# Kernel tuning notes

Hardware: AMD Instinct MI355X
Metric: run time of the kernel (lower is better)

## Reference

```python
import jax, jax.numpy as jnp
import numpy as np

# dims: M scalars (0e), K vectors (1e) in input; T = tp_features; N = batch of atoms
M, K, T, N = 128, 64, 64, 131072
D_IN = M + 3 * K  # 320, e3nn layout: [128x0e | 64x1e flattened as (mul, 3)]


def _act_norm(f):
    # e3nn Activation normalizes act so E_{z~N(0,1)}[act(z)^2] = 1
    z = np.linspace(-8.0, 8.0, 20001)
    pdf = np.exp(-0.5 * z * z) / np.sqrt(2.0 * np.pi)
    return float(np.sqrt(np.trapz(f(z) ** 2 * pdf, z)))

C_SILU = _act_norm(lambda z: z / (1.0 + np.exp(-z)))
C_RELU = _act_norm(lambda z: np.maximum(z, 0.0))
INV_SQRT_M = float(1.0 / np.sqrt(M))
INV_SQRT_K = float(1.0 / np.sqrt(K))
INV_SQRT_3 = float(1.0 / np.sqrt(3.0))  # wigner_3j(1,1,0) = delta_ij/sqrt(3)
TP_NORM = float(1.0 / np.sqrt(2.0 * T * T))  # fan-in over the 2 paths into 0e


def setup_inputs() -> dict:
    key = jax.random.key(0)
    ks = jax.random.split(key, 11)
    f32 = jnp.float32
    return {
        "x": jax.random.normal(ks[0], (N, D_IN), f32),
        "input_shift": jnp.zeros((D_IN,), f32),
        "output_scale": jnp.ones((), f32),
        # PerceptronLayer 1: Linear (Mx0e+Kx1e) -> ((M+K)x0e + Kx1e)
        "w0_1": jax.random.normal(ks[1], (M, M + K), f32),
        "b0_1": jnp.zeros((M + K,), f32),
        "w1_1": jax.random.normal(ks[2], (K, K), f32),
        # PerceptronLayer 2 (same irreps, resnet applies)
        "w0_2": jax.random.normal(ks[3], (M, M + K), f32),
        "b0_2": jnp.zeros((M + K,), f32),
        "w1_2": jax.random.normal(ks[4], (K, K), f32),
        # linear_out: (Mx0e+Kx1e) -> (Tx0e+Tx1e)
        "w0_o": jax.random.normal(ks[5], (M, T), f32),
        "b0_o": jnp.zeros((T,), f32),
        "w1_o": jax.random.normal(ks[6], (K, T), f32),
        # FullyConnectedTensorProduct (tp, tp) -> 1x0e: paths 0e*0e->0e, 1e*1e->0e
        "w_tp0": jax.random.normal(ks[7], (T, T), f32),
        "w_tp1": jax.random.normal(ks[8], (T, T), f32),
    }


def _linear(xs, xv, w0, b0, w1):
    # e3nn o3.Linear: per-irrep dense mixing with 1/sqrt(fan_in), bias on 0e only
    ys = xs @ w0 * INV_SQRT_M + b0          # [N, M+K] scalars + gates
    yv = jnp.einsum('nki,kj->nji', xv, w1) * INV_SQRT_K  # [N, K, 3]
    return ys, yv


def _gate(ys, yv):
    # e3nn Gate: silu on 0e scalars, relu on 0e gates, gate the 1e vectors
    s = jax.nn.silu(ys[:, :M]) / C_SILU     # [N, M]
    g = jax.nn.relu(ys[:, M:]) / C_RELU     # [N, K]
    return s, yv * g[:, :, None]


def reference(x, input_shift, output_scale,
              w0_1, b0_1, w1_1, w0_2, b0_2, w1_2,
              w0_o, b0_o, w1_o, w_tp0, w_tp1):
    x = x - input_shift
    xs = x[:, :M]                           # [N, M] 0e block
    xv = x[:, M:].reshape(-1, K, 3)         # [N, K, 3] 1e block
    for (w0, b0, w1) in ((w0_1, b0_1, w1_1), (w0_2, b0_2, w1_2)):
        ys, yv = _linear(xs, xv, w0, b0, w1)
        s, v = _gate(ys, yv)
        xs = xs + s                         # resnet: irreps_in == irreps_out
        xv = xv + v
    # linear_out -> irreps_tp = Tx0e + Tx1e
    zs = xs @ w0_o * INV_SQRT_M + b0_o                    # [N, T]
    zv = jnp.einsum('nki,kj->nji', xv, w1_o) * INV_SQRT_K # [N, T, 3]
    # FullyConnectedTensorProduct(z, z) -> 0e (avoid [N,T,T] blowup)
    y0 = jnp.sum((zs @ w_tp0) * zs, axis=-1)                                    # [N]
    y1 = jnp.sum(jnp.einsum('nui,uv->nvi', zv, w_tp1) * zv, axis=(1, 2)) * INV_SQRT_3
    y = (y0 + y1) * TP_NORM / output_scale
    return y[:, None]
```

## Files before the change

kernel.cpp:

```cpp
#include <hip/hip_runtime.h>
#include <math.h>


typedef _Float16 f16;
typedef _Float16 f16x8 __attribute__((ext_vector_type(8)));
typedef __fp16   fp16x2 __attribute__((ext_vector_type(2)));
typedef float    f32x4 __attribute__((ext_vector_type(4)));
typedef int      i32x4 __attribute__((ext_vector_type(4)));

#define MFMA16(a, b, c) __builtin_amdgcn_mfma_f32_16x16x32_f16(a, b, c, 0, 0, 0)

constexpr float INV_SQRT_M = 0.08838834764831845f;
constexpr float INV_SQRT_K = 0.125f;
constexpr float INV_SQRT_3 = 0.57735026918962576f;
constexpr float TP_NORM    = 0.011048543456039806f;

#define OFF_W01 0
#define OFF_W11 24576
#define OFF_W02 28672
#define OFF_W12 53248
#define OFF_W0O 57344
#define OFF_W1O 65536
#define OFF_TP0 69632
#define OFF_TP1 73728
#define PACK_UNITS 9728

#define LDS_W1   24576
#define LDS_W0O  0
#define LDS_W1O  8192
#define LDS_TP0  12288
#define LDS_TP1  16384

#define NTHR 512

__global__ void init_consts_kernel(float* __restrict__ ws) {
    __shared__ double red[256];
    const int t = threadIdx.x;
    double acc_s = 0.0, acc_r = 0.0;
    for (int i = t; i <= 20000; i += 256) {
        const double z = -8.0 + (16.0 * (double)i) / 20000.0;
        const double pdf = exp(-0.5 * z * z) / 2.5066282746310002;
        const double sil = z / (1.0 + exp(-z));
        const double wgt = (i == 0 || i == 20000) ? 0.5 : 1.0;
        acc_s += wgt * sil * sil * pdf;
        if (z > 0.0) acc_r += wgt * z * z * pdf;
    }
    red[t] = acc_s;
    __syncthreads();
    for (int o = 128; o > 0; o >>= 1) { if (t < o) red[t] += red[t + o]; __syncthreads(); }
    const double tot_s = red[0];
    __syncthreads();
    red[t] = acc_r;
    __syncthreads();
    for (int o = 128; o > 0; o >>= 1) { if (t < o) red[t] += red[t + o]; __syncthreads(); }
    if (t == 0) {
        const double dz = 16.0 / 20000.0;
        ws[0] = (float)(1.0 / sqrt(tot_s * dz));
        ws[1] = (float)(1.0 / sqrt(red[0] * dz));
    }
}

__global__ void pack_weights(const float* __restrict__ w01, const float* __restrict__ w11,
                             const float* __restrict__ w02, const float* __restrict__ w12,
                             const float* __restrict__ w0o, const float* __restrict__ w1o,
                             const float* __restrict__ tp0, const float* __restrict__ tp1,
                             f16* __restrict__ dst) {
    int u = blockIdx.x * 256 + threadIdx.x;
    if (u >= PACK_UNITS) return;
    const float* src; int NC, base, lu = u; float sc;
    if      (lu < 3072) {            src = w01; NC = 192; base = OFF_W01; sc = INV_SQRT_M; }
    else if (lu < 3584) { lu -= 3072; src = w11; NC = 64;  base = OFF_W11; sc = INV_SQRT_K; }
    else if (lu < 6656) { lu -= 3584; src = w02; NC = 192; base = OFF_W02; sc = INV_SQRT_M; }
    else if (lu < 7168) { lu -= 6656; src = w12; NC = 64;  base = OFF_W12; sc = INV_SQRT_K; }
    else if (lu < 8192) { lu -= 7168; src = w0o; NC = 64;  base = OFF_W0O; sc = INV_SQRT_M; }
    else if (lu < 8704) { lu -= 8192; src = w1o; NC = 64;  base = OFF_W1O; sc = INV_SQRT_K; }
    else if (lu < 9216) { lu -= 8704; src = tp0; NC = 64;  base = OFF_TP0; sc = 1.0f; }
    else                { lu -= 9216; src = tp1; NC = 64;  base = OFF_TP1; sc = INV_SQRT_3; }
    const int lane = lu & 63;
    const int frag = lu >> 6;
    const int NT = NC >> 4;
    const int kstep = frag / NT, nj = frag - kstep * NT;
    const int gl  = lane >> 4;
    const int col = nj * 16 + (lane & 15);
    f16 tmp[8];
    #pragma unroll
    for (int e = 0; e < 8; ++e) {
        const int row = kstep * 32 + ((e >> 2) << 4) + (gl << 2) + (e & 3);
        tmp[e] = (f16)(src[(size_t)row * NC + col] * sc);
    }
    *(f16x8*)&dst[(size_t)(base) + (size_t)lu * 8] = *(f16x8*)tmp;
}

__device__ __forceinline__ int pk2i(float a, float b) {
    union { fp16x2 h; int i; } u;
    u.h = __builtin_amdgcn_cvt_pkrtz(a, b);
    return u.i;
}

__device__ __forceinline__ f16x8 packB(f32x4 t0, f32x4 t1) {
    union { i32x4 i; f16x8 v; } u;
    u.i[0] = pk2i(t0[0], t0[1]);
    u.i[1] = pk2i(t0[2], t0[3]);
    u.i[2] = pk2i(t1[0], t1[1]);
    u.i[3] = pk2i(t1[2], t1[3]);
    return u.v;
}

union Frag { f16x8 v; fp16x2 h2[4]; };

__device__ __forceinline__ void resblock32(
    Frag (&xsS)[2][4], Frag (&xvS)[2][3][2],
    const f16* lds, const float* __restrict__ b0,
    float invCS, float invCR, int l, int g)
{
    f16x8 xsB[2][4];
    #pragma unroll
    for (int h = 0; h < 2; ++h)
        #pragma unroll
        for (int ks = 0; ks < 4; ++ks)
            xsB[h][ks] = xsS[h][ks].v;

    float gate[2][4][4];
    #pragma unroll
    for (int nj = 0; nj < 12; ++nj) {
        f32x4 acc0 = {0.f, 0.f, 0.f, 0.f}, acc1 = {0.f, 0.f, 0.f, 0.f};
        #pragma unroll
        for (int ks = 0; ks < 4; ++ks) {
            const f16x8 a = *(const f16x8*)&lds[(size_t)((ks * 12 + nj) * 64 + l) * 8];
            acc0 = MFMA16(a, xsB[0][ks], acc0);
            acc1 = MFMA16(a, xsB[1][ks], acc1);
        }
        const f32x4 bias = *(const f32x4*)(b0 + nj * 16 + g * 4);
        #pragma unroll
        for (int h = 0; h < 2; ++h) {
            const f32x4 acc = h ? acc1 : acc0;
            if (nj < 8) {
                float s[4];
                #pragma unroll
                for (int r = 0; r < 4; ++r) {
                    const float ys = acc[r] + bias[r];
                    s[r] = ys * __builtin_amdgcn_rcpf(1.0f + __expf(-ys)) * invCS;
                }
                xsS[h][nj >> 1].h2[2 * (nj & 1)]     += __builtin_amdgcn_cvt_pkrtz(s[0], s[1]);
                xsS[h][nj >> 1].h2[2 * (nj & 1) + 1] += __builtin_amdgcn_cvt_pkrtz(s[2], s[3]);
            } else {
                #pragma unroll
                for (int r = 0; r < 4; ++r) {
                    const float ys = acc[r] + bias[r];
                    gate[h][nj - 8][r] = fmaxf(ys, 0.f) * invCR;
                }
            }
        }
    }

    f16x8 xvB[2][3][2];
    #pragma unroll
    for (int h = 0; h < 2; ++h)
        #pragma unroll
        for (int i = 0; i < 3; ++i)
            #pragma unroll
            for (int ks = 0; ks < 2; ++ks)
                xvB[h][i][ks] = xvS[h][i][ks].v;

    #pragma unroll
    for (int i = 0; i < 3; ++i)
        #pragma unroll
        for (int nj = 0; nj < 4; ++nj) {
            f32x4 acc0 = {0.f, 0.f, 0.f, 0.f}, acc1 = {0.f, 0.f, 0.f, 0.f};
            #pragma unroll
            for (int ks = 0; ks < 2; ++ks) {
                const f16x8 a = *(const f16x8*)&lds[LDS_W1 + (size_t)((ks * 4 + nj) * 64 + l) * 8];
                acc0 = MFMA16(a, xvB[0][i][ks], acc0);
                acc1 = MFMA16(a, xvB[1][i][ks], acc1);
            }
            #pragma unroll
            for (int h = 0; h < 2; ++h) {
                const f32x4 acc = h ? acc1 : acc0;
                float u[4];
                #pragma unroll
                for (int r = 0; r < 4; ++r)
                    u[r] = acc[r] * gate[h][nj][r];
                xvS[h][i][nj >> 1].h2[2 * (nj & 1)]     += __builtin_amdgcn_cvt_pkrtz(u[0], u[1]);
                xvS[h][i][nj >> 1].h2[2 * (nj & 1) + 1] += __builtin_amdgcn_cvt_pkrtz(u[2], u[3]);
            }
        }
}

__global__ __launch_bounds__(NTHR, 2)
void corrnet_lds(const float* __restrict__ x, const float* __restrict__ shift,
                 const float* __restrict__ oscale,
                 const float* __restrict__ b01, const float* __restrict__ b02,
                 const float* __restrict__ b0o,
                 const f16* __restrict__ wp, const float* __restrict__ consts,
                 float* __restrict__ out)
{
    __shared__ __align__(16) f16 smem[3584 * 8];

    const int t = threadIdx.x;
    const int l = t & 63;
    const int w = __builtin_amdgcn_readfirstlane(t >> 6);
    const int g = l >> 4;
    const int c = l & 15;
    const size_t n0 = (size_t)blockIdx.x * 256 + (size_t)w * 32;

    const float invCS = consts[0], invCR = consts[1];
    const float inv_os = 1.0f / oscale[0];

    #pragma unroll
    for (int it = 0; it < 7; ++it) {
        const int u = it * NTHR + t;
        *(f16x8*)&smem[(size_t)u * 8] = *(const f16x8*)&wp[(size_t)u * 8];
    }

    Frag xsS[2][4];
    Frag xvS[2][3][2];
    #pragma unroll
    for (int h = 0; h < 2; ++h) {
        const float* xrow = x + (n0 + h * 16 + c) * 320;
        #pragma unroll
        for (int ks = 0; ks < 4; ++ks) {
            const int col = ks * 32 + g * 4;
            const f32x4 t0 = *(const f32x4*)(xrow + col)      - *(const f32x4*)(shift + col);
            const f32x4 t1 = *(const f32x4*)(xrow + col + 16) - *(const f32x4*)(shift + col + 16);
            xsS[h][ks].v = packB(t0, t1);
        }
        f32x4 tmp[3][4];
        #pragma unroll
        for (int tau = 0; tau < 4; ++tau) {
            const int col = 128 + 3 * (tau * 16 + g * 4);
            const f32x4 a0 = *(const f32x4*)(xrow + col)     - *(const f32x4*)(shift + col);
            const f32x4 a1 = *(const f32x4*)(xrow + col + 4) - *(const f32x4*)(shift + col + 4);
            const f32x4 a2 = *(const f32x4*)(xrow + col + 8) - *(const f32x4*)(shift + col + 8);
            float arr[12];
            #pragma unroll
            for (int e = 0; e < 4; ++e) {
                arr[e] = a0[e]; arr[4 + e] = a1[e]; arr[8 + e] = a2[e];
            }
            #pragma unroll
            for (int r = 0; r < 4; ++r)
                #pragma unroll
                for (int i = 0; i < 3; ++i)
                    tmp[i][tau][r] = arr[3 * r + i];
        }
        #pragma unroll
        for (int i = 0; i < 3; ++i)
            #pragma unroll
            for (int ks = 0; ks < 2; ++ks)
                xvS[h][i][ks].v = packB(tmp[i][2 * ks], tmp[i][2 * ks + 1]);
    }

    __syncthreads();
    resblock32(xsS, xvS, smem, b01, invCS, invCR, l, g);
    __syncthreads();

    #pragma unroll
    for (int it = 0; it < 7; ++it) {
        const int u = it * NTHR + t;
        *(f16x8*)&smem[(size_t)u * 8] = *(const f16x8*)&wp[(size_t)(OFF_W02) + (size_t)u * 8];
    }
    __syncthreads();
    resblock32(xsS, xvS, smem, b02, invCS, invCR, l, g);
    __syncthreads();

    #pragma unroll
    for (int it = 0; it < 5; ++it) {
        const int u = it * NTHR + t;
        *(f16x8*)&smem[(size_t)u * 8] = *(const f16x8*)&wp[(size_t)(OFF_W0O) + (size_t)u * 8];
    }
    __syncthreads();

    f32x4 zs[2][4];
    #pragma unroll
    for (int nj = 0; nj < 4; ++nj) {
        f32x4 acc0 = {0.f, 0.f, 0.f, 0.f}, acc1 = {0.f, 0.f, 0.f, 0.f};
        #pragma unroll
        for (int ks = 0; ks < 4; ++ks) {
            const f16x8 a = *(const f16x8*)&smem[LDS_W0O + (size_t)((ks * 4 + nj) * 64 + l) * 8];
            acc0 = MFMA16(a, xsS[0][ks].v, acc0);
            acc1 = MFMA16(a, xsS[1][ks].v, acc1);
        }
        const f32x4 bias = *(const f32x4*)(b0o + nj * 16 + g * 4);
        #pragma unroll
        for (int r = 0; r < 4; ++r) {
            zs[0][nj][r] = acc0[r] + bias[r];
            zs[1][nj][r] = acc1[r] + bias[r];
        }
    }

    float part[2]  = {0.f, 0.f};
    float part1[2] = {0.f, 0.f};

    {
        f16x8 zsB[2][2];
        #pragma unroll
        for (int h = 0; h < 2; ++h)
            #pragma unroll
            for (int ks = 0; ks < 2; ++ks)
                zsB[h][ks] = packB(zs[h][2 * ks], zs[h][2 * ks + 1]);
        #pragma unroll
        for (int nj = 0; nj < 4; ++nj) {
            f32x4 acc0 = {0.f, 0.f, 0.f, 0.f}, acc1 = {0.f, 0.f, 0.f, 0.f};
            #pragma unroll
            for (int ks = 0; ks < 2; ++ks) {
                const f16x8 a = *(const f16x8*)&smem[LDS_TP0 + (size_t)((ks * 4 + nj) * 64 + l) * 8];
                acc0 = MFMA16(a, zsB[0][ks], acc0);
                acc1 = MFMA16(a, zsB[1][ks], acc1);
            }
            #pragma unroll
            for (int r = 0; r < 4; ++r) {
                part[0] += acc0[r] * zs[0][nj][r];
                part[1] += acc1[r] * zs[1][nj][r];
            }
        }
    }

    #pragma unroll
    for (int i = 0; i < 3; ++i) {
        f32x4 zv[2][4];
        #pragma unroll
        for (int nj = 0; nj < 4; ++nj) {
            f32x4 acc0 = {0.f, 0.f, 0.f, 0.f}, acc1 = {0.f, 0.f, 0.f, 0.f};
            #pragma unroll
            for (int ks = 0; ks < 2; ++ks) {
                const f16x8 a = *(const f16x8*)&smem[LDS_W1O + (size_t)((ks * 4 + nj) * 64 + l) * 8];
                acc0 = MFMA16(a, xvS[0][i][ks].v, acc0);
                acc1 = MFMA16(a, xvS[1][i][ks].v, acc1);
            }
            #pragma unroll
            for (int r = 0; r < 4; ++r) {
                zv[0][nj][r] = acc0[r];
                zv[1][nj][r] = acc1[r];
            }
        }
        f16x8 zvB[2][2];
        #pragma unroll
        for (int h = 0; h < 2; ++h)
            #pragma unroll
            for (int ks = 0; ks < 2; ++ks)
                zvB[h][ks] = packB(zv[h][2 * ks], zv[h][2 * ks + 1]);
        #pragma unroll
        for (int nj = 0; nj < 4; ++nj) {
            f32x4 acc0 = {0.f, 0.f, 0.f, 0.f}, acc1 = {0.f, 0.f, 0.f, 0.f};
            #pragma unroll
            for (int ks = 0; ks < 2; ++ks) {
                const f16x8 a = *(const f16x8*)&smem[LDS_TP1 + (size_t)((ks * 4 + nj) * 64 + l) * 8];
                acc0 = MFMA16(a, zvB[0][ks], acc0);
                acc1 = MFMA16(a, zvB[1][ks], acc1);
            }
            #pragma unroll
            for (int r = 0; r < 4; ++r) {
                part1[0] += acc0[r] * zv[0][nj][r];
                part1[1] += acc1[r] * zv[1][nj][r];
            }
        }
    }
    #pragma unroll
    for (int h = 0; h < 2; ++h)
        part[h] += part1[h];

    #pragma unroll
    for (int h = 0; h < 2; ++h) {
        part[h] += __shfl_xor(part[h], 16, 64);
        part[h] += __shfl_xor(part[h], 32, 64);
    }

    if (l < 16)
        out[n0 + l] = part[0] * TP_NORM * inv_os;
    else if (l < 32)
        out[n0 + 16 + (l - 16)] = part[1] * TP_NORM * inv_os;
}

extern "C" void kernel_launch(void* const* d_in, const int* in_sizes, int n_in,
                              void* d_out, int out_size, void* d_ws, size_t ws_size,
                              hipStream_t stream) {
    const float* x      = (const float*)d_in[0];
    const float* shift  = (const float*)d_in[1];
    const float* oscale = (const float*)d_in[2];
    const float* w01    = (const float*)d_in[3];
    const float* b01    = (const float*)d_in[4];
    const float* w11    = (const float*)d_in[5];
    const float* w02    = (const float*)d_in[6];
    const float* b02    = (const float*)d_in[7];
    const float* w12    = (const float*)d_in[8];
    const float* w0o    = (const float*)d_in[9];
    const float* b0o    = (const float*)d_in[10];
    const float* w1o    = (const float*)d_in[11];
    const float* wtp0   = (const float*)d_in[12];
    const float* wtp1   = (const float*)d_in[13];
    float* out    = (float*)d_out;
    float* consts = (float*)d_ws;
    f16*   wp     = (f16*)((char*)d_ws + 16);

    init_consts_kernel<<<1, 256, 0, stream>>>(consts);
    pack_weights<<<(PACK_UNITS + 255) / 256, 256, 0, stream>>>(
        w01, w11, w02, w12, w0o, w1o, wtp0, wtp1, wp);

    const int nblocks = 131072 / 256;
    corrnet_lds<<<nblocks, NTHR, 0, stream>>>(
        x, shift, oscale, b01, b02, b0o, wp, consts, out);
}
```

Baseline: 91.13 us.

## Stage input rows through swizzled LDS with coalesced block-wide loads

Replaces per-lane strided global reads of x, where each lane read scattered 16-byte chunks of its own row, with a loop over 8 chunks of 32 rows. All 512 threads load each chunk into an XOR-swizzled LDS tile, and the owning wave then reads its fragments from LDS. This aims at full global-load coalescing and fewer wasted memory transactions. In exchange it serializes loading into 8 steps with two block barriers each, so only one wave consumes per step and global latency overlaps less.

```diff
diff --git a/kernel.cpp b/kernel.cpp
--- a/kernel.cpp
+++ b/kernel.cpp
@@ -32,6 +32,7 @@
 #define LDS_TP1  16384
 
 #define NTHR 512
+#define XSTR 324
 
 __global__ void init_consts_kernel(float* __restrict__ ws) {
     __shared__ double red[256];
@@ -195,60 +196,82 @@
                  float* __restrict__ out)
 {
     __shared__ __align__(16) f16 smem[3584 * 8];
+    float* smemF = (float*)smem;
 
     const int t = threadIdx.x;
     const int l = t & 63;
     const int w = __builtin_amdgcn_readfirstlane(t >> 6);
     const int g = l >> 4;
     const int c = l & 15;
-    const size_t n0 = (size_t)blockIdx.x * 256 + (size_t)w * 32;
+    const size_t nblk = (size_t)blockIdx.x * 256;
+    const size_t n0 = nblk + (size_t)w * 32;
 
     const float invCS = consts[0], invCR = consts[1];
     const float inv_os = 1.0f / oscale[0];
+
+    Frag xsS[2][4];
+    Frag xvS[2][3][2];
+    {
+        const int key = (c & 7) << 2;
+        #pragma unroll 1
+        for (int p = 0; p < 8; ++p) {
+            const float* xbase = x + (nblk + (size_t)p * 32) * 320;
+            #pragma unroll
+            for (int it = 0; it < 5; ++it) {
+                const int q    = it * NTHR + t;
+                const int row  = q / 80;
+                const int col4 = (q - row * 80) * 4;
+                const f32x4 v = *(const f32x4*)(xbase + row * 320 + col4)
+                              - *(const f32x4*)(shift + col4);
+                const int scol = col4 ^ ((row & 7) << 2);
+                *(f32x4*)&smemF[row * XSTR + scol] = v;
+            }
+            __syncthreads();
+            if (w == p) {
+                #pragma unroll
+                for (int h = 0; h < 2; ++h) {
+                    const int rbase = (h * 16 + c) * XSTR;
+                    #pragma unroll
+                    for (int ks = 0; ks < 4; ++ks) {
+                        const int col = ks * 32 + g * 4;
+                        const f32x4 t0 = *(const f32x4*)&smemF[rbase + (col ^ key)];
+                        const f32x4 t1 = *(const f32x4*)&smemF[rbase + ((col + 16) ^ key)];
+                        xsS[h][ks].v = packB(t0, t1);
+                    }
+                    f32x4 tmp[3][4];
+                    #pragma unroll
+                    for (int tau = 0; tau < 4; ++tau) {
+                        const int col0 = 128 + 3 * (tau * 16 + g * 4);
+                        const f32x4 a0 = *(const f32x4*)&smemF[rbase + (col0 ^ key)];
+                        const f32x4 a1 = *(const f32x4*)&smemF[rbase + ((col0 + 4) ^ key)];
+                        const f32x4 a2 = *(const f32x4*)&smemF[rbase + ((col0 + 8) ^ key)];
+                        float arr[12];
+                        #pragma unroll
+                        for (int e = 0; e < 4; ++e) {
+                            arr[e] = a0[e]; arr[4 + e] = a1[e]; arr[8 + e] = a2[e];
+                        }
+                        #pragma unroll
+                        for (int r = 0; r < 4; ++r)
+                            #pragma unroll
+                            for (int i = 0; i < 3; ++i)
+                                tmp[i][tau][r] = arr[3 * r + i];
+                    }
+                    #pragma unroll
+                    for (int i = 0; i < 3; ++i)
+                        #pragma unroll
+                        for (int ks = 0; ks < 2; ++ks)
+                            xvS[h][i][ks].v = packB(tmp[i][2 * ks], tmp[i][2 * ks + 1]);
+                }
+            }
+            __syncthreads();
+        }
+    }
 
     #pragma unroll
     for (int it = 0; it < 7; ++it) {
         const int u = it * NTHR + t;
         *(f16x8*)&smem[(size_t)u * 8] = *(const f16x8*)&wp[(size_t)u * 8];
     }
-
-    Frag xsS[2][4];
-    Frag xvS[2][3][2];
-    #pragma unroll
-    for (int h = 0; h < 2; ++h) {
-        const float* xrow = x + (n0 + h * 16 + c) * 320;
-        #pragma unroll
-        for (int ks = 0; ks < 4; ++ks) {
-            const int col = ks * 32 + g * 4;
-            const f32x4 t0 = *(const f32x4*)(xrow + col)      - *(const f32x4*)(shift + col);
-            const f32x4 t1 = *(const f32x4*)(xrow + col + 16) - *(const f32x4*)(shift + col + 16);
-            xsS[h][ks].v = packB(t0, t1);
-        }
-        f32x4 tmp[3][4];
-        #pragma unroll
-        for (int tau = 0; tau < 4; ++tau) {
-            const int col = 128 + 3 * (tau * 16 + g * 4);
-            const f32x4 a0 = *(const f32x4*)(xrow + col)     - *(const f32x4*)(shift + col);
-            const f32x4 a1 = *(const f32x4*)(xrow + col + 4) - *(const f32x4*)(shift + col + 4);
-            const f32x4 a2 = *(const f32x4*)(xrow + col + 8) - *(const f32x4*)(shift + col + 8);
-            float arr[12];
-            #pragma unroll
-            for (int e = 0; e < 4; ++e) {
-                arr[e] = a0[e]; arr[4 + e] = a1[e]; arr[8 + e] = a2[e];
-            }
-            #pragma unroll
-            for (int r = 0; r < 4; ++r)
-                #pragma unroll
-                for (int i = 0; i < 3; ++i)
-                    tmp[i][tau][r] = arr[3 * r + i];
-        }
-        #pragma unroll
-        for (int i = 0; i < 3; ++i)
-            #pragma unroll
-            for (int ks = 0; ks < 2; ++ks)
-                xvS[h][i][ks].v = packB(tmp[i][2 * ks], tmp[i][2 * ks + 1]);
-    }
-
     __syncthreads();
     resblock32(xsS, xvS, smem, b01, invCS, invCR, l, g);
     __syncthreads();
```

New measurement: 92.18 us. No clear change (+1.2%).

## Stage biases in LDS and widen constant-init kernel to 1024 threads

Applied to the files above, without the earlier changes.

Biases are packed into the workspace by the pack kernel and copied into shared memory alongside each weight stage, so the per-tile bias reads in the MFMA epilogues hit LDS instead of global memory. The init_consts kernel now uses 1024 threads, cutting its serial loop length. This adds a small LDS footprint and some extra copy instructions. The LDS bias region must not overlap the weight regions still in use.

```diff
diff --git a/kernel.cpp b/kernel.cpp
--- a/kernel.cpp
+++ b/kernel.cpp
@@ -24,20 +24,26 @@
 #define OFF_TP0 69632
 #define OFF_TP1 73728
 #define PACK_UNITS 9728
-
-#define LDS_W1   24576
-#define LDS_W0O  0
-#define LDS_W1O  8192
-#define LDS_TP0  12288
-#define LDS_TP1  16384
+#define FB01 38912
+#define FB02 39104
+#define FB0O 39296
+#define TOTAL_UNITS (PACK_UNITS + 448)
+
+#define LDS_W1     24576
+#define LDS_BIAS_F 14336
+#define LDS_W0O    0
+#define LDS_W1O    8192
+#define LDS_TP0    12288
+#define LDS_TP1    16384
+#define LDS_B0O_F  10240
 
 #define NTHR 512
 
 __global__ void init_consts_kernel(float* __restrict__ ws) {
-    __shared__ double red[256];
+    __shared__ double red[1024];
     const int t = threadIdx.x;
     double acc_s = 0.0, acc_r = 0.0;
-    for (int i = t; i <= 20000; i += 256) {
+    for (int i = t; i <= 20000; i += 1024) {
         const double z = -8.0 + (16.0 * (double)i) / 20000.0;
         const double pdf = exp(-0.5 * z * z) / 2.5066282746310002;
         const double sil = z / (1.0 + exp(-z));
@@ -47,12 +53,12 @@
     }
     red[t] = acc_s;
     __syncthreads();
-    for (int o = 128; o > 0; o >>= 1) { if (t < o) red[t] += red[t + o]; __syncthreads(); }
+    for (int o = 512; o > 0; o >>= 1) { if (t < o) red[t] += red[t + o]; __syncthreads(); }
     const double tot_s = red[0];
     __syncthreads();
     red[t] = acc_r;
     __syncthreads();
-    for (int o = 128; o > 0; o >>= 1) { if (t < o) red[t] += red[t + o]; __syncthreads(); }
+    for (int o = 512; o > 0; o >>= 1) { if (t < o) red[t] += red[t + o]; __syncthreads(); }
     if (t == 0) {
         const double dz = 16.0 / 20000.0;
         ws[0] = (float)(1.0 / sqrt(tot_s * dz));
@@ -64,9 +70,19 @@
                              const float* __restrict__ w02, const float* __restrict__ w12,
                              const float* __restrict__ w0o, const float* __restrict__ w1o,
                              const float* __restrict__ tp0, const float* __restrict__ tp1,
+                             const float* __restrict__ b01, const float* __restrict__ b02,
+                             const float* __restrict__ b0o,
                              f16* __restrict__ dst) {
     int u = blockIdx.x * 256 + threadIdx.x;
-    if (u >= PACK_UNITS) return;
+    if (u >= TOTAL_UNITS) return;
+    if (u >= PACK_UNITS) {
+        const int idx = u - PACK_UNITS;
+        float* dstF = (float*)dst;
+        if (idx < 192)      dstF[FB01 + idx] = b01[idx];
+        else if (idx < 384) dstF[FB02 + (idx - 192)] = b02[idx - 192];
+        else                dstF[FB0O + (idx - 384)] = b0o[idx - 384];
+        return;
+    }
     const float* src; int NC, base, lu = u; float sc;
     if      (lu < 3072) {            src = w01; NC = 192; base = OFF_W01; sc = INV_SQRT_M; }
     else if (lu < 3584) { lu -= 3072; src = w11; NC = 64;  base = OFF_W11; sc = INV_SQRT_K; }
@@ -110,9 +126,10 @@
 
 __device__ __forceinline__ void resblock32(
     Frag (&xsS)[2][4], Frag (&xvS)[2][3][2],
-    const f16* lds, const float* __restrict__ b0,
-    float invCS, float invCR, int l, int g)
+    const f16* lds, float invCS, float invCR, int l, int g)
 {
+    const float* biasF = (const float*)lds + LDS_BIAS_F;
+
     f16x8 xsB[2][4];
     #pragma unroll
     for (int h = 0; h < 2; ++h)
@@ -130,7 +147,7 @@
             acc0 = MFMA16(a, xsB[0][ks], acc0);
             acc1 = MFMA16(a, xsB[1][ks], acc1);
         }
-        const f32x4 bias = *(const f32x4*)(b0 + nj * 16 + g * 4);
+        const f32x4 bias = *(const f32x4*)&biasF[nj * 16 + g * 4];
         #pragma unroll
         for (int h = 0; h < 2; ++h) {
             const f32x4 acc = h ? acc1 : acc0;
@@ -189,12 +206,12 @@
 __global__ __launch_bounds__(NTHR, 2)
 void corrnet_lds(const float* __restrict__ x, const float* __restrict__ shift,
                  const float* __restrict__ oscale,
-                 const float* __restrict__ b01, const float* __restrict__ b02,
-                 const float* __restrict__ b0o,
                  const f16* __restrict__ wp, const float* __restrict__ consts,
                  float* __restrict__ out)
 {
-    __shared__ __align__(16) f16 smem[3584 * 8];
+    __shared__ __align__(16) f16 smem[29056];
+    float* smemF = (float*)smem;
+    const float* wpF = (const float*)wp;
 
     const int t = threadIdx.x;
     const int l = t & 63;
@@ -211,6 +228,8 @@
         const int u = it * NTHR + t;
         *(f16x8*)&smem[(size_t)u * 8] = *(const f16x8*)&wp[(size_t)u * 8];
     }
+    if (t < 48)
+        ((f32x4*)&smemF[LDS_BIAS_F])[t] = ((const f32x4*)&wpF[FB01])[t];
 
     Frag xsS[2][4];
     Frag xvS[2][3][2];
@@ -250,7 +269,7 @@
     }
 
     __syncthreads();
-    resblock32(xsS, xvS, smem, b01, invCS, invCR, l, g);
+    resblock32(xsS, xvS, smem, invCS, invCR, l, g);
     __syncthreads();
 
     #pragma unroll
@@ -258,8 +277,10 @@
         const int u = it * NTHR + t;
         *(f16x8*)&smem[(size_t)u * 8] = *(const f16x8*)&wp[(size_t)(OFF_W02) + (size_t)u * 8];
     }
-    __syncthreads();
-    resblock32(xsS, xvS, smem, b02, invCS, invCR, l, g);
+    if (t < 48)
+        ((f32x4*)&smemF[LDS_BIAS_F])[t] = ((const f32x4*)&wpF[FB02])[t];
+    __syncthreads();
+    resblock32(xsS, xvS, smem, invCS, invCR, l, g);
     __syncthreads();
 
     #pragma unroll
@@ -267,6 +288,8 @@
         const int u = it * NTHR + t;
         *(f16x8*)&smem[(size_t)u * 8] = *(const f16x8*)&wp[(size_t)(OFF_W0O) + (size_t)u * 8];
     }
+    if (t < 16)
+        ((f32x4*)&smemF[LDS_B0O_F])[t] = ((const f32x4*)&wpF[FB0O])[t];
     __syncthreads();
 
     f32x4 zs[2][4];
@@ -279,7 +302,7 @@
             acc0 = MFMA16(a, xsS[0][ks].v, acc0);
             acc1 = MFMA16(a, xsS[1][ks].v, acc1);
         }
-        const f32x4 bias = *(const f32x4*)(b0o + nj * 16 + g * 4);
+        const f32x4 bias = *(const f32x4*)&smemF[LDS_B0O_F + nj * 16 + g * 4];
         #pragma unroll
         for (int r = 0; r < 4; ++r) {
             zs[0][nj][r] = acc0[r] + bias[r];
@@ -391,11 +414,11 @@
     float* consts = (float*)d_ws;
     f16*   wp     = (f16*)((char*)d_ws + 16);
 
-    init_consts_kernel<<<1, 256, 0, stream>>>(consts);
-    pack_weights<<<(PACK_UNITS + 255) / 256, 256, 0, stream>>>(
-        w01, w11, w02, w12, w0o, w1o, wtp0, wtp1, wp);
+    init_consts_kernel<<<1, 1024, 0, stream>>>(consts);
+    pack_weights<<<(TOTAL_UNITS + 255) / 256, 256, 0, stream>>>(
+        w01, w11, w02, w12, w0o, w1o, wtp0, wtp1, b01, b02, b0o, wp);
 
     const int nblocks = 131072 / 256;
     corrnet_lds<<<nblocks, NTHR, 0, stream>>>(
-        x, shift, oscale, b01, b02, b0o, wp, consts, out);
-}
+        x, shift, oscale, wp, consts, out);
+}
```

Result: faster. 75.65 us (-17.0%).
